# Kernel optimization log

Measured on AMD Instinct MI355X. Metric: run time of the kernel, lower is better.

Reference implementation:

```python
import jax, jax.numpy as jnp
import numpy as np

NUM_BINS = 256


def _equalize_channel(chan):
    # chan: (P,) int32 pixel values in [0, 255]. PIL/torchvision-style equalize.
    hist = jnp.zeros(NUM_BINS, jnp.float32).at[chan].add(1.0)
    total = hist.sum()
    # value of the last nonzero histogram bin (excluded from step computation)
    nz = hist > 0
    last_idx = (NUM_BINS - 1) - jnp.argmax(nz[::-1])
    last = hist[last_idx]
    step = jnp.floor((total - last) / 255.0)
    cum = jnpp_cumsum = jnp.cumsum(hist)
    lut = jnp.floor((cum + jnp.floor(step / 2.0)) / jnp.maximum(step, 1.0))
    # shift right by one (pad a leading 0, drop last) and clamp to [0,255]
    lut = jnp.clip(jnp.concatenate([jnp.zeros(1, jnp.float32), lut[:-1]]), 0.0, 255.0)
    ident = jnp.arange(NUM_BINS, dtype=jnp.float32)
    lut = jnp.where(step == 0, ident, lut)  # step==0 -> identity mapping
    return lut[chan]


def _equalize(x):
    # x: (N, C, H, W) float, pixel values -> uint8 semantics
    N, C, H, W = x.shape
    xi = jnp.clip(x, 0, 255).astype(jnp.int32).reshape(N * C, H * W)
    out = jax.vmap(_equalize_channel)(xi)  # (N*C, H*W) float32
    return out.reshape(N, C, H, W).astype(x.dtype)


def setup_inputs() -> dict:
    key = jax.random.key(0)
    x = jax.random.uniform(key, (64, 3, 512, 512), dtype=jnp.float32) * 255.0
    magnitude = 5
    return {"x": x, "magnitude": magnitude}


def reference(x, magnitude):
    # magnitude is unused in the original forward (Equalize ignores it)
    return _equalize(x)
```

## Files before the change

### kernel.cpp

```cpp
#include <hip/hip_runtime.h>

#define NBINS 256
#define NCHAN 192
#define HIST_BPC 8
#define APPLY_BPC 16
#define TPB 256
#define VEC_PER_CHAN (512 * 512 / 4)
#define NCOPY 32

__global__ __launch_bounds__(TPB) void hist_pack(const float* __restrict__ x,
                                                 unsigned* __restrict__ packed,
                                                 int* __restrict__ partials) {
    __shared__ int lh[NBINS * NCOPY];
    const int chan = blockIdx.x / HIST_BPC;
    const int blk  = blockIdx.x % HIST_BPC;
    const int tid  = threadIdx.x;
    const int cp   = (tid & 63) >> 1;

    for (int i = tid; i < NBINS * NCOPY; i += TPB) lh[i] = 0;
    __syncthreads();

    const int vecPerBlock = VEC_PER_CHAN / HIST_BPC;
    const size_t base = (size_t)chan * VEC_PER_CHAN + blk * vecPerBlock;
    const float4* bx = (const float4*)x + base;
    unsigned* bp = packed + base;

    for (int i = tid; i < vecPerBlock; i += TPB) {
        float4 v = bx[i];
        int a = (int)fminf(fmaxf(v.x, 0.f), 255.f);
        int b = (int)fminf(fmaxf(v.y, 0.f), 255.f);
        int c = (int)fminf(fmaxf(v.z, 0.f), 255.f);
        int d = (int)fminf(fmaxf(v.w, 0.f), 255.f);
        bp[i] = (unsigned)(a | (b << 8) | (c << 16) | (d << 24));
        atomicAdd(&lh[(a << 5) + cp], 1);
        atomicAdd(&lh[(b << 5) + cp], 1);
        atomicAdd(&lh[(c << 5) + cp], 1);
        atomicAdd(&lh[(d << 5) + cp], 1);
    }
    __syncthreads();

    int s = 0;
    #pragma unroll
    for (int k = 0; k < NCOPY; ++k) s += lh[(tid << 5) + ((tid + k) & 31)];
    partials[(chan * HIST_BPC + blk) * NBINS + tid] = s;
}

__global__ __launch_bounds__(TPB) void apply_kernel(const unsigned* __restrict__ packed,
                                                    float* __restrict__ out,
                                                    const int* __restrict__ partials) {
    __shared__ int scan[NBINS];
    __shared__ float slut[NBINS * NCOPY];
    __shared__ int s_last_idx, s_last;

    const int chan = blockIdx.x / APPLY_BPC;
    const int blk  = blockIdx.x % APPLY_BPC;
    const int tid  = threadIdx.x;
    const int cp   = (tid & 63) >> 1;

    int h = 0;
    #pragma unroll
    for (int b = 0; b < HIST_BPC; ++b)
        h += partials[(chan * HIST_BPC + b) * NBINS + tid];
    scan[tid] = h;
    if (tid == 0) s_last_idx = 0;
    __syncthreads();
    if (h > 0) atomicMax(&s_last_idx, tid);

    for (int off = 1; off < NBINS; off <<= 1) {
        __syncthreads();
        int t = (tid >= off) ? scan[tid - off] : 0;
        __syncthreads();
        scan[tid] += t;
    }
    __syncthreads();
    if (tid == s_last_idx) s_last = h;
    __syncthreads();

    const int total = scan[NBINS - 1];
    const int step  = (total - s_last) / 255;

    float lutv;
    if (step == 0)      lutv = (float)tid;
    else if (tid == 0)  lutv = 0.f;
    else {
        int l = (scan[tid - 1] + (step >> 1)) / step;
        lutv = (float)(l < 255 ? l : 255);
    }
    #pragma unroll
    for (int k = 0; k < NCOPY; ++k) slut[(tid << 5) + ((tid + k) & 31)] = lutv;
    __syncthreads();

    const int vecPerBlock = VEC_PER_CHAN / APPLY_BPC;
    const size_t base = (size_t)chan * VEC_PER_CHAN + blk * vecPerBlock;
    const unsigned* bp = packed + base;
    float4* bo = (float4*)out + base;

    for (int i = tid; i < vecPerBlock; i += TPB) {
        unsigned p = bp[i];
        float4 o;
        o.x = slut[(int)((p & 255u) << 5) + cp];
        o.y = slut[(int)(((p >> 8) & 255u) << 5) + cp];
        o.z = slut[(int)(((p >> 16) & 255u) << 5) + cp];
        o.w = slut[(int)((p >> 24) << 5) + cp];
        bo[i] = o;
    }
}

extern "C" void kernel_launch(void* const* d_in, const int* in_sizes, int n_in,
                              void* d_out, int out_size, void* d_ws, size_t ws_size,
                              hipStream_t stream) {
    const float* x = (const float*)d_in[0];
    float* out = (float*)d_out;

    unsigned* packed = (unsigned*)d_ws;
    int* partials = (int*)d_ws + (size_t)NCHAN * VEC_PER_CHAN;

    hist_pack<<<NCHAN * HIST_BPC, TPB, 0, stream>>>(x, packed, partials);
    apply_kernel<<<NCHAN * APPLY_BPC, TPB, 0, stream>>>(packed, out, partials);
}
```

Measured before the change: 375.7 us.

## Drop packed byte buffer; re-read input in apply and split out LUT kernel

Removes the intermediate packed uint8 buffer, so the apply pass re-reads the float input and recomputes the clamped bin indices. The per-channel LUT is computed once in a separate small kernel instead of in every apply block. It also halves the shared-memory histogram/LUT copies, halves apply blocks per channel, and uses nontemporal stores. Total DRAM traffic rises unless the second input read hits cache, and the fewer copies raise atomic contention.

```diff
diff --git a/kernel.cpp b/kernel.cpp
--- a/kernel.cpp
+++ b/kernel.cpp
@@ -3,59 +3,54 @@
 #define NBINS 256
 #define NCHAN 192
 #define HIST_BPC 8
-#define APPLY_BPC 16
+#define APPLY_BPC 8
 #define TPB 256
 #define VEC_PER_CHAN (512 * 512 / 4)
-#define NCOPY 32
+#define NCOPY 16
 
-__global__ __launch_bounds__(TPB) void hist_pack(const float* __restrict__ x,
-                                                 unsigned* __restrict__ packed,
-                                                 int* __restrict__ partials) {
+typedef float f4 __attribute__((ext_vector_type(4)));
+
+__global__ __launch_bounds__(TPB) void hist_kernel(const float* __restrict__ x,
+                                                   int* __restrict__ partials) {
     __shared__ int lh[NBINS * NCOPY];
     const int chan = blockIdx.x / HIST_BPC;
     const int blk  = blockIdx.x % HIST_BPC;
     const int tid  = threadIdx.x;
-    const int cp   = (tid & 63) >> 1;
+    const int cp   = (tid & 63) >> 2;
 
     for (int i = tid; i < NBINS * NCOPY; i += TPB) lh[i] = 0;
     __syncthreads();
 
     const int vecPerBlock = VEC_PER_CHAN / HIST_BPC;
-    const size_t base = (size_t)chan * VEC_PER_CHAN + blk * vecPerBlock;
-    const float4* bx = (const float4*)x + base;
-    unsigned* bp = packed + base;
+    const size_t base = (size_t)chan * VEC_PER_CHAN + (size_t)blk * vecPerBlock;
+    const f4* bx = (const f4*)x + base;
 
+    #pragma unroll 4
     for (int i = tid; i < vecPerBlock; i += TPB) {
-        float4 v = bx[i];
+        f4 v = bx[i];
         int a = (int)fminf(fmaxf(v.x, 0.f), 255.f);
         int b = (int)fminf(fmaxf(v.y, 0.f), 255.f);
         int c = (int)fminf(fmaxf(v.z, 0.f), 255.f);
         int d = (int)fminf(fmaxf(v.w, 0.f), 255.f);
-        bp[i] = (unsigned)(a | (b << 8) | (c << 16) | (d << 24));
-        atomicAdd(&lh[(a << 5) + cp], 1);
-        atomicAdd(&lh[(b << 5) + cp], 1);
-        atomicAdd(&lh[(c << 5) + cp], 1);
-        atomicAdd(&lh[(d << 5) + cp], 1);
+        atomicAdd(&lh[(a << 4) + cp], 1);
+        atomicAdd(&lh[(b << 4) + cp], 1);
+        atomicAdd(&lh[(c << 4) + cp], 1);
+        atomicAdd(&lh[(d << 4) + cp], 1);
     }
     __syncthreads();
 
     int s = 0;
     #pragma unroll
-    for (int k = 0; k < NCOPY; ++k) s += lh[(tid << 5) + ((tid + k) & 31)];
+    for (int k = 0; k < NCOPY; ++k) s += lh[(tid << 4) + ((tid + k) & 15)];
     partials[(chan * HIST_BPC + blk) * NBINS + tid] = s;
 }
 
-__global__ __launch_bounds__(TPB) void apply_kernel(const unsigned* __restrict__ packed,
-                                                    float* __restrict__ out,
-                                                    const int* __restrict__ partials) {
+__global__ __launch_bounds__(TPB) void lut_kernel(const int* __restrict__ partials,
+                                                  float* __restrict__ lut) {
     __shared__ int scan[NBINS];
-    __shared__ float slut[NBINS * NCOPY];
     __shared__ int s_last_idx, s_last;
-
-    const int chan = blockIdx.x / APPLY_BPC;
-    const int blk  = blockIdx.x % APPLY_BPC;
+    const int chan = blockIdx.x;
     const int tid  = threadIdx.x;
-    const int cp   = (tid & 63) >> 1;
 
     int h = 0;
     #pragma unroll
@@ -86,23 +81,41 @@
         int l = (scan[tid - 1] + (step >> 1)) / step;
         lutv = (float)(l < 255 ? l : 255);
     }
+    lut[chan * NBINS + tid] = lutv;
+}
+
+__global__ __launch_bounds__(TPB) void apply_kernel(const float* __restrict__ x,
+                                                    float* __restrict__ out,
+                                                    const float* __restrict__ lut) {
+    __shared__ float slut[NBINS * NCOPY];
+    const int chan = blockIdx.x / APPLY_BPC;
+    const int blk  = blockIdx.x % APPLY_BPC;
+    const int tid  = threadIdx.x;
+    const int cp   = (tid & 63) >> 2;
+
+    const float lv = lut[chan * NBINS + tid];
     #pragma unroll
-    for (int k = 0; k < NCOPY; ++k) slut[(tid << 5) + ((tid + k) & 31)] = lutv;
+    for (int k = 0; k < NCOPY; ++k) slut[(tid << 4) + ((tid + k) & 15)] = lv;
     __syncthreads();
 
     const int vecPerBlock = VEC_PER_CHAN / APPLY_BPC;
-    const size_t base = (size_t)chan * VEC_PER_CHAN + blk * vecPerBlock;
-    const unsigned* bp = packed + base;
-    float4* bo = (float4*)out + base;
+    const size_t base = (size_t)chan * VEC_PER_CHAN + (size_t)blk * vecPerBlock;
+    const f4* bx = (const f4*)x + base;
+    f4* bo = (f4*)out + base;
 
+    #pragma unroll 4
     for (int i = tid; i < vecPerBlock; i += TPB) {
-        unsigned p = bp[i];
-        float4 o;
-        o.x = slut[(int)((p & 255u) << 5) + cp];
-        o.y = slut[(int)(((p >> 8) & 255u) << 5) + cp];
-        o.z = slut[(int)(((p >> 16) & 255u) << 5) + cp];
-        o.w = slut[(int)((p >> 24) << 5) + cp];
-        bo[i] = o;
+        f4 v = bx[i];
+        int a = (int)fminf(fmaxf(v.x, 0.f), 255.f);
+        int b = (int)fminf(fmaxf(v.y, 0.f), 255.f);
+        int c = (int)fminf(fmaxf(v.z, 0.f), 255.f);
+        int d = (int)fminf(fmaxf(v.w, 0.f), 255.f);
+        f4 o;
+        o.x = slut[(a << 4) + cp];
+        o.y = slut[(b << 4) + cp];
+        o.z = slut[(c << 4) + cp];
+        o.w = slut[(d << 4) + cp];
+        __builtin_nontemporal_store(o, &bo[i]);
     }
 }
 
@@ -112,9 +125,10 @@
     const float* x = (const float*)d_in[0];
     float* out = (float*)d_out;
 
-    unsigned* packed = (unsigned*)d_ws;
-    int* partials = (int*)d_ws + (size_t)NCHAN * VEC_PER_CHAN;
+    int* partials = (int*)d_ws;
+    float* lut = (float*)((int*)d_ws + (size_t)NCHAN * HIST_BPC * NBINS);
 
-    hist_pack<<<NCHAN * HIST_BPC, TPB, 0, stream>>>(x, packed, partials);
-    apply_kernel<<<NCHAN * APPLY_BPC, TPB, 0, stream>>>(packed, out, partials);
+    hist_kernel<<<NCHAN * HIST_BPC, TPB, 0, stream>>>(x, partials);
+    lut_kernel<<<NCHAN, TPB, 0, stream>>>(partials, lut);
+    apply_kernel<<<NCHAN * APPLY_BPC, TPB, 0, stream>>>(x, out, lut);
 }
```

Result: no change. 370.9 us (-1.3%).
